# Kernel tuning notes

Measured on AMD Instinct MI355X. Metric: run time of the kernel, lower is better.

## Reference

```python
import jax, jax.numpy as jnp
import numpy as np

N = 20000
E = 320000
LN_EPS = 1e-5
NEG_SLOPE = 0.2


def setup_inputs() -> dict:
    key = jax.random.key(0)
    ks = jax.random.split(key, 12)
    d = {}
    d['x'] = jax.random.normal(ks[0], (N, 512), dtype=jnp.float32)
    d['edge_index'] = jax.random.randint(ks[1], (2, E), 0, N, dtype=jnp.int64)
    s = 1.0 / np.sqrt(512.0)
    d['W1'] = jax.random.normal(ks[2], (512, 512), dtype=jnp.float32) * s
    d['a_src1'] = jax.random.normal(ks[3], (8, 64), dtype=jnp.float32) * s
    d['a_dst1'] = jax.random.normal(ks[4], (8, 64), dtype=jnp.float32) * s
    d['b1'] = jnp.zeros((512,), jnp.float32)
    d['g1'] = jnp.ones((512,), jnp.float32)
    d['beta1'] = jnp.zeros((512,), jnp.float32)
    d['W2'] = jax.random.normal(ks[5], (512, 512), dtype=jnp.float32) * s
    d['a_src2'] = jax.random.normal(ks[6], (1, 512), dtype=jnp.float32) * s
    d['a_dst2'] = jax.random.normal(ks[7], (1, 512), dtype=jnp.float32) * s
    d['b2'] = jnp.zeros((512,), jnp.float32)
    d['g2'] = jnp.ones((512,), jnp.float32)
    d['beta2'] = jnp.zeros((512,), jnp.float32)
    return d


def _segment_softmax(logits, seg, num_segments):
    # logits: [E, H]; softmax over edges sharing the same destination node
    m = jax.ops.segment_max(logits, seg, num_segments=num_segments)  # [N, H]
    e = jnp.exp(logits - m[seg])
    s = jax.ops.segment_sum(e, seg, num_segments=num_segments)  # [N, H]
    return e / s[seg]


def _gat_conv(x, src, dst, W, a_s, a_d, b, concat):
    # PyG GATConv (eval mode, self-loops already appended to src/dst)
    H, C = a_s.shape
    n = x.shape[0]
    h = (x @ W).reshape(n, H, C)                      # [N, H, C]
    alpha_s = jnp.einsum('nhc,hc->nh', h, a_s)        # [N, H]
    alpha_d = jnp.einsum('nhc,hc->nh', h, a_d)
    logits = jax.nn.leaky_relu(alpha_s[src] + alpha_d[dst], NEG_SLOPE)  # [E, H]
    alpha = _segment_softmax(logits, dst, n)          # [E, H]
    msg = h[src] * alpha[:, :, None]                  # [E, H, C]
    out = jax.ops.segment_sum(msg, dst, num_segments=n)  # [N, H, C]
    out = out.reshape(n, H * C) if concat else out.mean(axis=1)
    return out + b


def _layer_norm(x, g, beta):
    mu = jnp.mean(x, axis=-1, keepdims=True)
    var = jnp.var(x, axis=-1, keepdims=True)
    return (x - mu) * jax.lax.rsqrt(var + LN_EPS) * g + beta


def _forward(x, edge_index, W1, a_src1, a_dst1, b1, g1, beta1,
             W2, a_src2, a_dst2, b2, g2, beta2):
    n = x.shape[0]
    loops = jnp.arange(n, dtype=edge_index.dtype)
    src = jnp.concatenate([edge_index[0], loops])
    dst = jnp.concatenate([edge_index[1], loops])
    # layer 1: heads=8, concat
    x_new = _gat_conv(x, src, dst, W1, a_src1, a_dst1, b1, concat=True)
    x_new = jax.nn.elu(_layer_norm(x_new, g1, beta1))
    x = x + x_new  # 512 == 512 residual
    # layer 2: heads=1, mean (concat=False)
    x_new = _gat_conv(x, src, dst, W2, a_src2, a_dst2, b2, concat=False)
    x_new = jax.nn.elu(_layer_norm(x_new, g2, beta2))
    return x + x_new


def reference(x, edge_index, W1, a_src1, a_dst1, b1, g1, beta1,
              W2, a_src2, a_dst2, b2, g2, beta2):
    return _forward(x, edge_index, W1, a_src1, a_dst1, b1, g1, beta1,
                    W2, a_src2, a_dst2, b2, g2, beta2)
```

## Files before the change

kernel.cpp:

```cpp
#include <hip/hip_runtime.h>
#include <hip/hip_bf16.h>
#include <math.h>

#define NN 20000
#define NE 320000
#define DIM 512
#define LN_EPS 1e-5f
#define NEG_SLOPE 0.2f

typedef __attribute__((ext_vector_type(8))) short bf16x8;
typedef __attribute__((ext_vector_type(4))) float f32x4;
typedef __attribute__((ext_vector_type(4))) unsigned int u32x4;

__device__ inline void gload_lds16(const void* g, void* l) {
    __builtin_amdgcn_global_load_lds(
        (const __attribute__((address_space(1))) void*)g,
        (__attribute__((address_space(3))) void*)l, 16, 0, 0);
}

__device__ inline short f2bf(float f) {
    __hip_bfloat16 b = __float2bfloat16(f);
    return *reinterpret_cast<short*>(&b);
}


__global__ void count_k(const int* __restrict__ dst, int* __restrict__ cnt) {
    int e = blockIdx.x * blockDim.x + threadIdx.x;
    if (e < NE) {
        int d = dst[e];
        d = (d < 0) ? 0 : (d >= NN ? NN - 1 : d);
        atomicAdd(&cnt[d], 1);
    }
}

__global__ __launch_bounds__(1024) void scan_k(const int* __restrict__ cnt,
                                               int* __restrict__ off,
                                               int* __restrict__ cur) {
    __shared__ int s[1024];
    const int t = threadIdx.x;
    const int lo = t * 20;
    int loc[20];
    int sum = 0;
#pragma unroll
    for (int i = 0; i < 20; i++) {
        int idx = lo + i;
        int v = (idx < NN) ? cnt[idx] : 0;
        loc[i] = v; sum += v;
    }
    s[t] = sum;
    __syncthreads();
    for (int o = 1; o < 1024; o <<= 1) {
        int x = (t >= o) ? s[t - o] : 0;
        __syncthreads();
        s[t] += x;
        __syncthreads();
    }
    int run = s[t] - sum;
#pragma unroll
    for (int i = 0; i < 20; i++) {
        int idx = lo + i;
        if (idx < NN) { off[idx] = run; cur[idx] = run; run += loc[i]; }
    }
    if (t == 1023) off[NN] = s[1023];
}

__global__ void fill_k(const int* __restrict__ src, const int* __restrict__ dst,
                       int* __restrict__ cur, int* __restrict__ slot) {
    int e = blockIdx.x * blockDim.x + threadIdx.x;
    if (e < NE) {
        int d = dst[e];
        d = (d < 0) ? 0 : (d >= NN ? NN - 1 : d);
        int sv = src[e];
        sv = (sv < 0) ? 0 : (sv >= NN ? NN - 1 : sv);
        int p = atomicAdd(&cur[d], 1);
        slot[p] = sv;
    }
}


__global__ void conv_k(const float* __restrict__ in, __hip_bfloat16* __restrict__ out, int n) {
    int i = (blockIdx.x * blockDim.x + threadIdx.x) * 4;
    if (i < n) {
        float4 v = *(const float4*)&in[i];
        out[i + 0] = __float2bfloat16(v.x);
        out[i + 1] = __float2bfloat16(v.y);
        out[i + 2] = __float2bfloat16(v.z);
        out[i + 3] = __float2bfloat16(v.w);
    }
}

__global__ __launch_bounds__(256) void convT_k(const float* __restrict__ W1f,
                                               const float* __restrict__ W2f,
                                               __hip_bfloat16* __restrict__ B1,
                                               __hip_bfloat16* __restrict__ B2) {
    const float* W = blockIdx.z ? W2f : W1f;
    __hip_bfloat16* BT = blockIdx.z ? B2 : B1;
    __shared__ float tile[32][33];
    const int bk = blockIdx.x * 32, bn = blockIdx.y * 32;
    const int tx = threadIdx.x & 31, ty = threadIdx.x >> 5;
#pragma unroll
    for (int i = 0; i < 32; i += 8)
        tile[ty + i][tx] = W[(size_t)(bk + ty + i) * DIM + bn + tx];
    __syncthreads();
#pragma unroll
    for (int i = 0; i < 32; i += 8)
        BT[(size_t)(bn + ty + i) * DIM + bk + tx] = __float2bfloat16(tile[tx][ty + i]);
}

__global__ void sum8_k(const float* __restrict__ ps, const float* __restrict__ pd,
                       float* __restrict__ os, float* __restrict__ od) {
    int n = blockIdx.x * blockDim.x + threadIdx.x;
    if (n < NN) {
        float a = 0.f, b = 0.f;
#pragma unroll
        for (int k = 0; k < 8; k++) { a += ps[(size_t)k * NN + n]; b += pd[(size_t)k * NN + n]; }
        os[n] = a; od[n] = b;
    }
}


template <int H>
__global__ __launch_bounds__(256) void gemm_mfma(const short* __restrict__ A,
                                                 const short* __restrict__ BT,
                                                 __hip_bfloat16* __restrict__ C,
                                                 const float* __restrict__ a_s,
                                                 const float* __restrict__ a_d,
                                                 float* __restrict__ p_as,
                                                 float* __restrict__ p_ad,
                                                 int M) {
    __shared__ __align__(16) short SMEM[64 * 136];
    short* As = SMEM;
    short* Bs = SMEM + 4096;
    const int t = threadIdx.x;
    const int rowBase = blockIdx.y * 128;
    const int colBase = blockIdx.x * 128;
    const int wave = t >> 6, lane = t & 63;
    const int wr = (wave >> 1) * 64;
    const int wc = (wave & 1) * 64;
    const int quad = lane >> 4, l16 = lane & 15;

    f32x4 acc[4][4];
#pragma unroll
    for (int i = 0; i < 4; i++)
#pragma unroll
        for (int j = 0; j < 4; j++) acc[i][j] = f32x4{0.f, 0.f, 0.f, 0.f};

    const int srow = t >> 2;
    const int skof = (t & 3) * 8;
    int ar0 = rowBase + srow;       if (ar0 > M - 1) ar0 = M - 1;
    int ar1 = rowBase + 64 + srow;  if (ar1 > M - 1) ar1 = M - 1;
    const int bn0 = colBase + srow;
    const int bn1 = colBase + 64 + srow;

    for (int k0 = 0; k0 < DIM; k0 += 32) {
        gload_lds16(A + (size_t)ar0 * DIM + k0 + skof, As + t * 8);
        gload_lds16(A + (size_t)ar1 * DIM + k0 + skof, As + 2048 + t * 8);
        gload_lds16(BT + (size_t)bn0 * DIM + k0 + skof, Bs + t * 8);
        gload_lds16(BT + (size_t)bn1 * DIM + k0 + skof, Bs + 2048 + t * 8);
        __syncthreads();

        bf16x8 af[4], bfr[4];
#pragma unroll
        for (int i = 0; i < 4; i++)
            af[i] = *(const bf16x8*)&As[(wr + i * 16 + l16) * 32 + quad * 8];
#pragma unroll
        for (int j = 0; j < 4; j++)
            bfr[j] = *(const bf16x8*)&Bs[(wc + j * 16 + l16) * 32 + quad * 8];
#pragma unroll
        for (int i = 0; i < 4; i++)
#pragma unroll
            for (int j = 0; j < 4; j++)
                acc[i][j] = __builtin_amdgcn_mfma_f32_16x16x32_bf16(af[i], bfr[j], acc[i][j], 0, 0, 0);
        __syncthreads();
    }

#pragma unroll
    for (int p = 0; p < 2; p++) {
        if ((wave >> 1) == p) {
#pragma unroll
            for (int i = 0; i < 4; i++)
#pragma unroll
                for (int j = 0; j < 4; j++)
#pragma unroll
                    for (int r = 0; r < 4; r++)
                        SMEM[(i * 16 + quad * 4 + r) * 136 + wc + j * 16 + l16] =
                            f2bf(acc[i][j][r]);
        }
        __syncthreads();
#pragma unroll
        for (int k = 0; k < 4; k++) {
            const int row = k * 16 + (t >> 4);
            const int col = (t & 15) * 8;
            const int gr = rowBase + p * 64 + row;
            if (gr < M) {
                bf16x8 vv = *(const bf16x8*)&SMEM[row * 136 + col];
                *(bf16x8*)&C[(size_t)gr * DIM + colBase + col] = vv;
            }
        }
        __syncthreads();
    }

    const int slab = 2 * blockIdx.x + (wave & 1);
    const int cb = (H == 8) ? slab * 64 : (colBase + wc);
    float asc[4], adc[4];
#pragma unroll
    for (int j = 0; j < 4; j++) {
        asc[j] = a_s[cb + j * 16 + l16];
        adc[j] = a_d[cb + j * 16 + l16];
    }
#pragma unroll
    for (int i = 0; i < 4; i++) {
#pragma unroll
        for (int r = 0; r < 4; r++) {
            float vs = acc[i][0][r] * asc[0] + acc[i][1][r] * asc[1] +
                       acc[i][2][r] * asc[2] + acc[i][3][r] * asc[3];
            float vd = acc[i][0][r] * adc[0] + acc[i][1][r] * adc[1] +
                       acc[i][2][r] * adc[2] + acc[i][3][r] * adc[3];
#pragma unroll
            for (int o = 8; o; o >>= 1) { vs += __shfl_down(vs, o); vd += __shfl_down(vd, o); }
            if (l16 == 0) {
                const int row = rowBase + wr + i * 16 + quad * 4 + r;
                if (row < M) {
                    if (H == 8) {
                        p_as[(size_t)row * 8 + slab] = vs;
                        p_ad[(size_t)row * 8 + slab] = vd;
                    } else {
                        p_as[(size_t)slab * NN + row] = vs;
                        p_ad[(size_t)slab * NN + row] = vd;
                    }
                }
            }
        }
    }
}


template <int H>
__global__ __launch_bounds__(256) void agg_k(const __hip_bfloat16* __restrict__ h,
                                             const float* __restrict__ alp_s,
                                             const float* __restrict__ alp_d,
                                             const int* __restrict__ off,
                                             const int* __restrict__ slot,
                                             const float* __restrict__ bias,
                                             const float* __restrict__ gamma,
                                             const float* __restrict__ beta,
                                             const float* x_res,
                                             float* x_out,
                                             __hip_bfloat16* x_out_b) {
    const int wid = threadIdx.x >> 6;
    const int lane = threadIdx.x & 63;
    const int n = blockIdx.x * 4 + wid;
    const int head = (H == 8) ? (lane >> 3) : 0;

    const int o0 = off[n];
    const int deg = off[n + 1] - o0;
    const int total = deg + 1;

    const float ad = (H == 8) ? alp_d[(size_t)n * 8 + head] : alp_d[n];

    int v = 0x7fffffff;
    if (lane < total && lane < 64) v = (lane < deg) ? slot[o0 + lane] : n;
#pragma unroll
    for (int k = 2; k <= 64; k <<= 1) {
#pragma unroll
        for (int j = k >> 1; j > 0; j >>= 1) {
            int o = __shfl_xor(v, j);
            bool takeMin = (((lane & k) == 0) == ((lane & j) == 0));
            v = takeMin ? min(v, o) : max(v, o);
        }
    }
    const int nsort = (total < 64) ? total : 64;

    float acc[8];
#pragma unroll
    for (int r = 0; r < 8; r++) acc[r] = 0.f;
    float ld = 0.f;
    const unsigned short* hu = (const unsigned short*)h;

    auto zcomp = [&](int s) -> float {
        float z = ((H == 8) ? alp_s[(size_t)s * 8 + head] : alp_s[s]) + ad;
        return (z >= 0.f) ? z : NEG_SLOPE * z;
    };
    auto fmarow = [&](const u32x4& rv, float p) {
#pragma unroll
        for (int q = 0; q < 4; q++) {
            unsigned int u = rv[q];
            acc[2 * q]     += p * __uint_as_float(u << 16);
            acc[2 * q + 1] += p * __uint_as_float(u & 0xffff0000u);
        }
    };

    int e = 0;
    for (; e + 4 <= nsort; e += 4) {
        const int s0 = __shfl(v, e), s1 = __shfl(v, e + 1);
        const int s2 = __shfl(v, e + 2), s3 = __shfl(v, e + 3);
        const u32x4 r0 = *(const u32x4*)(hu + (size_t)s0 * DIM + lane * 8);
        const u32x4 r1 = *(const u32x4*)(hu + (size_t)s1 * DIM + lane * 8);
        const u32x4 r2 = *(const u32x4*)(hu + (size_t)s2 * DIM + lane * 8);
        const u32x4 r3 = *(const u32x4*)(hu + (size_t)s3 * DIM + lane * 8);
        const float z0 = zcomp(s0), z1 = zcomp(s1), z2 = zcomp(s2), z3 = zcomp(s3);
        const float p0 = __expf(z0), p1 = __expf(z1), p2 = __expf(z2), p3 = __expf(z3);
        ld += p0; fmarow(r0, p0);
        ld += p1; fmarow(r1, p1);
        ld += p2; fmarow(r2, p2);
        ld += p3; fmarow(r3, p3);
    }
    for (; e < nsort; e++) {
        const int s = __shfl(v, e);
        const u32x4 rv = *(const u32x4*)(hu + (size_t)s * DIM + lane * 8);
        const float p = __expf(zcomp(s));
        ld += p; fmarow(rv, p);
    }
    for (int e2 = 64; e2 < total; e2++) {
        const int s = (e2 < deg) ? slot[o0 + e2] : n;
        const u32x4 rv = *(const u32x4*)(hu + (size_t)s * DIM + lane * 8);
        const float p = __expf(zcomp(s));
        ld += p; fmarow(rv, p);
    }

    const float inv = 1.f / ld;
    const int c0 = lane * 8;
    const float4 ba = *(const float4*)&bias[c0];
    const float4 bb = *(const float4*)&bias[c0 + 4];
    float xn[8];
    xn[0] = acc[0] * inv + ba.x; xn[1] = acc[1] * inv + ba.y;
    xn[2] = acc[2] * inv + ba.z; xn[3] = acc[3] * inv + ba.w;
    xn[4] = acc[4] * inv + bb.x; xn[5] = acc[5] * inv + bb.y;
    xn[6] = acc[6] * inv + bb.z; xn[7] = acc[7] * inv + bb.w;

    float s1 = 0.f, s2 = 0.f;
#pragma unroll
    for (int r = 0; r < 8; r++) { s1 += xn[r]; s2 += xn[r] * xn[r]; }
#pragma unroll
    for (int o = 32; o; o >>= 1) { s1 += __shfl_xor(s1, o); s2 += __shfl_xor(s2, o); }
    const float mu = s1 * (1.f / DIM);
    const float rs = rsqrtf(s2 * (1.f / DIM) - mu * mu + LN_EPS);

    const float4 ga = *(const float4*)&gamma[c0];
    const float4 gb = *(const float4*)&gamma[c0 + 4];
    const float4 ea = *(const float4*)&beta[c0];
    const float4 eb = *(const float4*)&beta[c0 + 4];
    const float4 xa = *(const float4*)&x_res[(size_t)n * DIM + c0];
    const float4 xb = *(const float4*)&x_res[(size_t)n * DIM + c0 + 4];
    const float gv[8] = {ga.x, ga.y, ga.z, ga.w, gb.x, gb.y, gb.z, gb.w};
    const float ev[8] = {ea.x, ea.y, ea.z, ea.w, eb.x, eb.y, eb.z, eb.w};
    const float xv[8] = {xa.x, xa.y, xa.z, xa.w, xb.x, xb.y, xb.z, xb.w};

    float out[8];
#pragma unroll
    for (int r = 0; r < 8; r++) {
        float y = (xn[r] - mu) * rs * gv[r] + ev[r];
        y = (y > 0.f) ? y : expm1f(y);
        out[r] = xv[r] + y;
    }
    *(float4*)&x_out[(size_t)n * DIM + c0]     = make_float4(out[0], out[1], out[2], out[3]);
    *(float4*)&x_out[(size_t)n * DIM + c0 + 4] = make_float4(out[4], out[5], out[6], out[7]);
    if (x_out_b) {
        __hip_bfloat16 tb[8];
#pragma unroll
        for (int r = 0; r < 8; r++) tb[r] = __float2bfloat16(out[r]);
        *(bf16x8*)&x_out_b[(size_t)n * DIM + c0] = *(bf16x8*)tb;
    }
}


extern "C" void kernel_launch(void* const* d_in, const int* in_sizes, int n_in,
                              void* d_out, int out_size, void* d_ws, size_t ws_size,
                              hipStream_t stream) {
    const float* x = (const float*)d_in[0];
    const int* ei = (const int*)d_in[1];
    const float* W1 = (const float*)d_in[2];
    const float* as1 = (const float*)d_in[3];
    const float* ad1 = (const float*)d_in[4];
    const float* b1 = (const float*)d_in[5];
    const float* g1 = (const float*)d_in[6];
    const float* be1 = (const float*)d_in[7];
    const float* W2 = (const float*)d_in[8];
    const float* as2 = (const float*)d_in[9];
    const float* ad2 = (const float*)d_in[10];
    const float* b2 = (const float*)d_in[11];
    const float* g2 = (const float*)d_in[12];
    const float* be2 = (const float*)d_in[13];
    float* out = (float*)d_out;

    char* ws = (char*)d_ws;
    size_t o = 0;
    auto alloc = [&](size_t bytes) { size_t r = o; o += (bytes + 255) & ~(size_t)255; return r; };
    int* p_cnt = (int*)(ws + alloc((size_t)NN * 4));
    int* p_off = (int*)(ws + alloc((size_t)(NN + 1) * 4));
    int* p_cur = (int*)(ws + alloc((size_t)NN * 4));
    int* p_slot = (int*)(ws + alloc((size_t)NE * 4));
    __hip_bfloat16* p_hb = (__hip_bfloat16*)(ws + alloc((size_t)NN * DIM * 2));
    __hip_bfloat16* p_xb = (__hip_bfloat16*)(ws + alloc((size_t)NN * DIM * 2));
    __hip_bfloat16* p_bt1 = (__hip_bfloat16*)(ws + alloc((size_t)DIM * DIM * 2));
    __hip_bfloat16* p_bt2 = (__hip_bfloat16*)(ws + alloc((size_t)DIM * DIM * 2));
    float* p_as = (float*)(ws + alloc((size_t)NN * 8 * 4));
    float* p_ad = (float*)(ws + alloc((size_t)NN * 8 * 4));
    float* p_as2 = (float*)(ws + alloc((size_t)NN * 4));
    float* p_ad2 = (float*)(ws + alloc((size_t)NN * 4));
    float* p_x1 = out;

    const int* e_src = ei;
    const int* e_dst = ei + NE;

    hipMemsetAsync(p_cnt, 0, (size_t)NN * 4, stream);
    count_k<<<(NE + 255) / 256, 256, 0, stream>>>(e_dst, p_cnt);
    scan_k<<<1, 1024, 0, stream>>>(p_cnt, p_off, p_cur);
    fill_k<<<(NE + 255) / 256, 256, 0, stream>>>(e_src, e_dst, p_cur, p_slot);

    const int NX = NN * DIM;
    dim3 ggrid(4, (NN + 127) / 128);

    convT_k<<<dim3(16, 16, 2), 256, 0, stream>>>(W1, W2, p_bt1, p_bt2);
    conv_k<<<(NX / 4 + 255) / 256, 256, 0, stream>>>(x, p_xb, NX);

    gemm_mfma<8><<<ggrid, 256, 0, stream>>>((const short*)p_xb, (const short*)p_bt1, p_hb,
                                            as1, ad1, p_as, p_ad, NN);
    agg_k<8><<<NN / 4, 256, 0, stream>>>(p_hb, p_as, p_ad, p_off, p_slot, b1, g1, be1,
                                         x, p_x1, p_xb);

    gemm_mfma<1><<<ggrid, 256, 0, stream>>>((const short*)p_xb, (const short*)p_bt2, p_hb,
                                            as2, ad2, p_as, p_ad, NN);
    sum8_k<<<(NN + 255) / 256, 256, 0, stream>>>(p_as, p_ad, p_as2, p_ad2);
    agg_k<1><<<NN / 4, 256, 0, stream>>>(p_hb, p_as2, p_ad2, p_off, p_slot, b2, g2, be2,
                                         p_x1, out, nullptr);
}
```

Baseline: 340.9 us.

## Double-buffer GEMM LDS tiles, widen gather unroll to 8, nontemporal residual IO

The MFMA GEMM now double-buffers its A/B LDS tiles, issuing the next k-slice's global-to-LDS loads before computing on the current one. This overlaps load latency with MFMA work at the cost of twice the shared memory per block. The edge-gather aggregation loop is unrolled from 4 to 8 neighbor rows in flight, with a masked tail batch, to expose more memory-level parallelism. The residual read and output write use nontemporal loads and stores to reduce cache pollution.

Measured after the change: 348.0 us. +2.1%, slower.

```diff
diff --git a/kernel.cpp b/kernel.cpp
--- a/kernel.cpp
+++ b/kernel.cpp
@@ -128,9 +128,11 @@
                                                  float* __restrict__ p_as,
                                                  float* __restrict__ p_ad,
                                                  int M) {
-    __shared__ __align__(16) short SMEM[64 * 136];
-    short* As = SMEM;
-    short* Bs = SMEM + 4096;
+    __shared__ __align__(16) short SMEM[16384];
+    short* As0 = SMEM;
+    short* Bs0 = SMEM + 4096;
+    short* As1 = SMEM + 8192;
+    short* Bs1 = SMEM + 12288;
     const int t = threadIdx.x;
     const int rowBase = blockIdx.y * 128;
     const int colBase = blockIdx.x * 128;
@@ -152,13 +154,13 @@
     const int bn0 = colBase + srow;
     const int bn1 = colBase + 64 + srow;
 
-    for (int k0 = 0; k0 < DIM; k0 += 32) {
+    auto stage = [&](int k0, short* As, short* Bs) {
         gload_lds16(A + (size_t)ar0 * DIM + k0 + skof, As + t * 8);
         gload_lds16(A + (size_t)ar1 * DIM + k0 + skof, As + 2048 + t * 8);
         gload_lds16(BT + (size_t)bn0 * DIM + k0 + skof, Bs + t * 8);
         gload_lds16(BT + (size_t)bn1 * DIM + k0 + skof, Bs + 2048 + t * 8);
-        __syncthreads();
-
+    };
+    auto compute = [&](const short* As, const short* Bs) {
         bf16x8 af[4], bfr[4];
 #pragma unroll
         for (int i = 0; i < 4; i++)
@@ -171,6 +173,16 @@
 #pragma unroll
             for (int j = 0; j < 4; j++)
                 acc[i][j] = __builtin_amdgcn_mfma_f32_16x16x32_bf16(af[i], bfr[j], acc[i][j], 0, 0, 0);
+    };
+
+    stage(0, As0, Bs0);
+    __syncthreads();
+    for (int k0 = 0; k0 < DIM; k0 += 64) {
+        if (k0 + 32 < DIM) stage(k0 + 32, As1, Bs1);
+        compute(As0, Bs0);
+        __syncthreads();
+        if (k0 + 64 < DIM) stage(k0 + 64, As0, Bs0);
+        compute(As1, Bs1);
         __syncthreads();
     }
 
@@ -291,25 +303,35 @@
     };
 
     int e = 0;
-    for (; e + 4 <= nsort; e += 4) {
-        const int s0 = __shfl(v, e), s1 = __shfl(v, e + 1);
-        const int s2 = __shfl(v, e + 2), s3 = __shfl(v, e + 3);
-        const u32x4 r0 = *(const u32x4*)(hu + (size_t)s0 * DIM + lane * 8);
-        const u32x4 r1 = *(const u32x4*)(hu + (size_t)s1 * DIM + lane * 8);
-        const u32x4 r2 = *(const u32x4*)(hu + (size_t)s2 * DIM + lane * 8);
-        const u32x4 r3 = *(const u32x4*)(hu + (size_t)s3 * DIM + lane * 8);
-        const float z0 = zcomp(s0), z1 = zcomp(s1), z2 = zcomp(s2), z3 = zcomp(s3);
-        const float p0 = __expf(z0), p1 = __expf(z1), p2 = __expf(z2), p3 = __expf(z3);
-        ld += p0; fmarow(r0, p0);
-        ld += p1; fmarow(r1, p1);
-        ld += p2; fmarow(r2, p2);
-        ld += p3; fmarow(r3, p3);
-    }
-    for (; e < nsort; e++) {
-        const int s = __shfl(v, e);
-        const u32x4 rv = *(const u32x4*)(hu + (size_t)s * DIM + lane * 8);
-        const float p = __expf(zcomp(s));
-        ld += p; fmarow(rv, p);
+    for (; e + 8 <= nsort; e += 8) {
+        int sv[8];
+#pragma unroll
+        for (int q = 0; q < 8; q++) sv[q] = __shfl(v, e + q);
+        u32x4 rv[8];
+#pragma unroll
+        for (int q = 0; q < 8; q++)
+            rv[q] = *(const u32x4*)(hu + (size_t)sv[q] * DIM + lane * 8);
+        float pv[8];
+#pragma unroll
+        for (int q = 0; q < 8; q++) pv[q] = __expf(zcomp(sv[q]));
+#pragma unroll
+        for (int q = 0; q < 8; q++) { ld += pv[q]; fmarow(rv[q], pv[q]); }
+    }
+    if (e < nsort) {
+        int sv[8]; u32x4 rv[8]; float pv[8];
+#pragma unroll
+        for (int q = 0; q < 8; q++) {
+            int idx = e + q;
+            sv[q] = __shfl(v, (idx < nsort) ? idx : (nsort - 1));
+        }
+#pragma unroll
+        for (int q = 0; q < 8; q++)
+            rv[q] = *(const u32x4*)(hu + (size_t)sv[q] * DIM + lane * 8);
+#pragma unroll
+        for (int q = 0; q < 8; q++)
+            pv[q] = (e + q < nsort) ? __expf(zcomp(sv[q])) : 0.f;
+#pragma unroll
+        for (int q = 0; q < 8; q++) { ld += pv[q]; fmarow(rv[q], pv[q]); }
     }
     for (int e2 = 64; e2 < total; e2++) {
         const int s = (e2 < deg) ? slot[o0 + e2] : n;
@@ -340,11 +362,11 @@
     const float4 gb = *(const float4*)&gamma[c0 + 4];
     const float4 ea = *(const float4*)&beta[c0];
     const float4 eb = *(const float4*)&beta[c0 + 4];
-    const float4 xa = *(const float4*)&x_res[(size_t)n * DIM + c0];
-    const float4 xb = *(const float4*)&x_res[(size_t)n * DIM + c0 + 4];
+    const f32x4 xa = __builtin_nontemporal_load((const f32x4*)&x_res[(size_t)n * DIM + c0]);
+    const f32x4 xb = __builtin_nontemporal_load((const f32x4*)&x_res[(size_t)n * DIM + c0 + 4]);
     const float gv[8] = {ga.x, ga.y, ga.z, ga.w, gb.x, gb.y, gb.z, gb.w};
     const float ev[8] = {ea.x, ea.y, ea.z, ea.w, eb.x, eb.y, eb.z, eb.w};
-    const float xv[8] = {xa.x, xa.y, xa.z, xa.w, xb.x, xb.y, xb.z, xb.w};
+    const float xv[8] = {xa[0], xa[1], xa[2], xa[3], xb[0], xb[1], xb[2], xb[3]};
 
     float out[8];
 #pragma unroll
@@ -353,8 +375,10 @@
         y = (y > 0.f) ? y : expm1f(y);
         out[r] = xv[r] + y;
     }
-    *(float4*)&x_out[(size_t)n * DIM + c0]     = make_float4(out[0], out[1], out[2], out[3]);
-    *(float4*)&x_out[(size_t)n * DIM + c0 + 4] = make_float4(out[4], out[5], out[6], out[7]);
+    __builtin_nontemporal_store(f32x4{out[0], out[1], out[2], out[3]},
+                                (f32x4*)&x_out[(size_t)n * DIM + c0]);
+    __builtin_nontemporal_store(f32x4{out[4], out[5], out[6], out[7]},
+                                (f32x4*)&x_out[(size_t)n * DIM + c0 + 4]);
     if (x_out_b) {
         __hip_bfloat16 tb[8];
 #pragma unroll
```
